# Kernel tuning notes

Measured on AMD Instinct MI355X. Metric: run time of the kernel, lower is better.

## Reference

```python
import jax, jax.numpy as jnp
import numpy as np

N = 50000
E = 800000
F_IN = 128
HID = 128
NCLS = 40


def setup_inputs() -> dict:
    key = jax.random.key(0)
    ks = jax.random.split(key, 12)
    def glorot(k, fan_in, fan_out):
        s = jnp.sqrt(6.0 / (fan_in + fan_out))
        return jax.random.uniform(k, (fan_in, fan_out), jnp.float32, -s, s)
    x = jax.random.normal(ks[0], (N, F_IN), jnp.float32)
    edge_index = jax.random.randint(ks[1], (2, E), 0, N, jnp.int64)
    W1 = glorot(ks[2], F_IN, HID); b1 = jnp.zeros((HID,), jnp.float32)
    W2 = glorot(ks[3], HID, HID);  b2 = jnp.zeros((HID,), jnp.float32)
    W3 = glorot(ks[4], HID, HID);  b3 = jnp.zeros((HID,), jnp.float32)
    Wc = glorot(ks[5], HID, NCLS)
    bc = jnp.zeros((NCLS,), jnp.float32)
    return {"x": x, "edge_index": edge_index, "W1": W1, "b1": b1,
            "W2": W2, "b2": b2, "W3": W3, "b3": b3, "Wc": Wc, "bc": bc}


def _gcn_conv(h, src, dst, norm, W, b):
    # GCNConv: linear transform, then normalized scatter-add aggregation
    h = h @ W                              # [N, out]
    msg = h[src] * norm[:, None]           # [E+N, out] gathered + scaled
    out = jax.ops.segment_sum(msg, dst, num_segments=N)
    return out + b


def reference(x, edge_index, W1, b1, W2, b2, W3, b3, Wc, bc):
    # add self-loops (PyG GCNConv default) and compute symmetric norm once
    loop = jnp.arange(N, dtype=edge_index.dtype)
    src = jnp.concatenate([edge_index[0], loop])
    dst = jnp.concatenate([edge_index[1], loop])
    deg = jax.ops.segment_sum(jnp.ones_like(dst, dtype=x.dtype), dst, num_segments=N)
    dinv = jax.lax.rsqrt(deg)              # deg >= 1 due to self-loops
    norm = dinv[src] * dinv[dst]           # [E+N]

    h = jax.nn.relu(_gcn_conv(x, src, dst, norm, W1, b1))
    h = jax.nn.relu(_gcn_conv(h, src, dst, norm, W2, b2))
    h = jax.nn.relu(_gcn_conv(h, src, dst, norm, W3, b3))
    out = h @ Wc + bc
    return (out, h)
```

## Files before the change

kernel.cpp:

```cpp
#include <hip/hip_runtime.h>
#include <hip/hip_fp16.h>


#define FEAT 128

typedef _Float16 half_t;
typedef _Float16 f16x8 __attribute__((ext_vector_type(8)));
typedef float f32x16 __attribute__((ext_vector_type(16)));


__global__ __launch_bounds__(256) void k_prep(const float* __restrict__ W1,
                                              const float* __restrict__ W2,
                                              const float* __restrict__ W3,
                                              half_t* __restrict__ Wt1,
                                              half_t* __restrict__ Wt2,
                                              half_t* __restrict__ Wt3,
                                              int* __restrict__ deg, int N) {
  int idx = blockIdx.x * 256 + threadIdx.x;
  if (idx < N) deg[idx] = 0;
  if (idx < 3 * 16384) {
    int which = idx >> 14;
    int i = idx & 16383;
    int k = i >> 7, n = i & 127;
    const float* W = (which == 0) ? W1 : (which == 1) ? W2 : W3;
    half_t* Wt = (which == 0) ? Wt1 : (which == 1) ? Wt2 : Wt3;
    Wt[n * 128 + k] = (half_t)W[i];
  }
}


__global__ __launch_bounds__(256) void k_count_rank(const int* __restrict__ dst,
                                                    int* __restrict__ deg,
                                                    int* __restrict__ rank, int E) {
  int e = blockIdx.x * 256 + threadIdx.x;
  if (e < E) rank[e] = atomicAdd(&deg[dst[e]], 1);
}

__global__ __launch_bounds__(256) void k_scanA(const int* __restrict__ deg,
                                               int* __restrict__ partial, int N) {
  __shared__ int s[256];
  int t = threadIdx.x;
  int i = blockIdx.x * 256 + t;
  s[t] = (i < N) ? deg[i] : 0;
  __syncthreads();
  for (int off = 128; off > 0; off >>= 1) {
    if (t < off) s[t] += s[t + off];
    __syncthreads();
  }
  if (t == 0) partial[blockIdx.x] = s[0];
}

__global__ __launch_bounds__(256) void k_scanB(int* __restrict__ partial, int nblk,
                                               int* __restrict__ offsets, int N) {
  __shared__ int s[256];
  int t = threadIdx.x;
  int v = (t < nblk) ? partial[t] : 0;
  s[t] = v;
  __syncthreads();
  for (int off = 1; off < 256; off <<= 1) {
    int x = (t >= off) ? s[t - off] : 0;
    __syncthreads();
    s[t] += x;
    __syncthreads();
  }
  if (t < nblk) partial[t] = s[t] - v;
  if (t == 0) offsets[N] = s[255];
}

__global__ __launch_bounds__(256) void k_scanC(const int* __restrict__ deg,
                                               const int* __restrict__ partial,
                                               int* __restrict__ offsets,
                                               float* __restrict__ dinv, int N) {
  __shared__ int s[256];
  int t = threadIdx.x;
  int i = blockIdx.x * 256 + t;
  int v = (i < N) ? deg[i] : 0;
  s[t] = v;
  __syncthreads();
  for (int off = 1; off < 256; off <<= 1) {
    int x = (t >= off) ? s[t - off] : 0;
    __syncthreads();
    s[t] += x;
    __syncthreads();
  }
  if (i < N) {
    offsets[i] = partial[blockIdx.x] + s[t] - v;
    dinv[i] = rsqrtf((float)(v + 1));
  }
}

__global__ __launch_bounds__(256) void k_place(const int* __restrict__ src,
                                               const int* __restrict__ dst,
                                               const int* __restrict__ offsets,
                                               const int* __restrict__ rank,
                                               int* __restrict__ col, int E) {
  int e = blockIdx.x * 256 + threadIdx.x;
  if (e < E) col[offsets[dst[e]] + rank[e]] = src[e];
}

template <int SRC_FP32>
__global__ __launch_bounds__(256) void k_gemm_mfma(const void* __restrict__ Asrc,
                                                   const half_t* __restrict__ Wt,
                                                   const float* __restrict__ dinv,
                                                   half_t* __restrict__ T,
                                                   int nrows) {
  __shared__ char lds[65536];
  char* sA = lds;
  char* sW = lds + 32768;
  int t = threadIdx.x;
  int rowBase = blockIdx.x * 128;
  int rowsHere = min(128, nrows - rowBase);

  #pragma unroll
  for (int i = 0; i < 8; ++i) {
    int lin = t + i * 256;
    int r = lin >> 4, c = lin & 15;
    *(float4*)(sW + r * 256 + ((c * 16) ^ ((r & 15) << 4))) =
        *(const float4*)((const char*)Wt + r * 256 + c * 16);
  }
  if (SRC_FP32) {
    const float* Af = (const float*)Asrc;
    #pragma unroll
    for (int i = 0; i < 8; ++i) {
      int lin = t + i * 256;
      int r = lin >> 4, c = lin & 15;
      f16x8 h = {};
      if (r < rowsHere) {
        const float4* p = (const float4*)(Af + (size_t)(rowBase + r) * FEAT + c * 8);
        float4 v0 = p[0], v1 = p[1];
        h[0] = (half_t)v0.x; h[1] = (half_t)v0.y; h[2] = (half_t)v0.z; h[3] = (half_t)v0.w;
        h[4] = (half_t)v1.x; h[5] = (half_t)v1.y; h[6] = (half_t)v1.z; h[7] = (half_t)v1.w;
      }
      *(f16x8*)(sA + r * 256 + ((c * 16) ^ ((r & 15) << 4))) = h;
    }
  } else {
    const char* Ah = (const char*)Asrc;
    #pragma unroll
    for (int i = 0; i < 8; ++i) {
      int lin = t + i * 256;
      int r = lin >> 4, c = lin & 15;
      float4 v = {};
      if (r < rowsHere) v = *(const float4*)(Ah + (size_t)(rowBase + r) * 256 + c * 16);
      *(float4*)(sA + r * 256 + ((c * 16) ^ ((r & 15) << 4))) = v;
    }
  }
  __syncthreads();

  int wv = t >> 6;
  int l = t & 63;
  int l31 = l & 31;
  int lhi = l >> 5;
  int sw = (l31 & 15) << 4;

  f32x16 acc[4] = {};

  #pragma unroll
  for (int step = 0; step < 8; ++step) {
    int ko = (step * 32 + lhi * 16) ^ sw;
    f16x8 a  = *(const f16x8*)(sA + (wv * 32 + l31) * 256 + ko);
    f16x8 b0 = *(const f16x8*)(sW + (l31) * 256 + ko);
    f16x8 b1 = *(const f16x8*)(sW + (32 + l31) * 256 + ko);
    f16x8 b2 = *(const f16x8*)(sW + (64 + l31) * 256 + ko);
    f16x8 b3 = *(const f16x8*)(sW + (96 + l31) * 256 + ko);
    acc[0] = __builtin_amdgcn_mfma_f32_32x32x16_f16(a, b0, acc[0], 0, 0, 0);
    acc[1] = __builtin_amdgcn_mfma_f32_32x32x16_f16(a, b1, acc[1], 0, 0, 0);
    acc[2] = __builtin_amdgcn_mfma_f32_32x32x16_f16(a, b2, acc[2], 0, 0, 0);
    acc[3] = __builtin_amdgcn_mfma_f32_32x32x16_f16(a, b3, acc[3], 0, 0, 0);
  }

  #pragma unroll
  for (int j = 0; j < 16; ++j) {
    int rloc = wv * 32 + (j & 3) + 8 * (j >> 2) + 4 * lhi;
    if (rloc < rowsHere) {
      int grow = rowBase + rloc;
      float d = dinv[grow];
      #pragma unroll
      for (int n = 0; n < 4; ++n) {
        T[(size_t)grow * FEAT + n * 32 + l31] = (half_t)(acc[n][j] * d);
      }
    }
  }
}

template <int OUTF>
__global__ __launch_bounds__(256) void k_aggregate(const uint2* __restrict__ T4,
                                                   const int* __restrict__ offsets,
                                                   const int* __restrict__ col,
                                                   const float* __restrict__ dinv,
                                                   const float* __restrict__ bias,
                                                   float4* __restrict__ outF,
                                                   uint2* __restrict__ outH,
                                                   int N) {
  int wave = threadIdx.x >> 6;
  int half = (threadIdx.x >> 5) & 1;
  int q = threadIdx.x & 31;
  int node = (blockIdx.x * 4 + wave) * 2 + half;
  if (node >= N) return;
  int e0 = offsets[node], e1 = offsets[node + 1];

  uint2 sv = T4[(size_t)node * 32 + q];
  __half2 h0 = *(__half2*)&sv.x, h1 = *(__half2*)&sv.y;
  float ax = __half2float(h0.x), ay = __half2float(h0.y);
  float az = __half2float(h1.x), aw = __half2float(h1.y);

  int e = e0;
  for (; e + 8 <= e1; e += 8) {
    int s0 = col[e + 0], s1 = col[e + 1], s2 = col[e + 2], s3 = col[e + 3];
    int s4 = col[e + 4], s5 = col[e + 5], s6 = col[e + 6], s7 = col[e + 7];
    uint2 v0 = T4[(size_t)s0 * 32 + q];
    uint2 v1 = T4[(size_t)s1 * 32 + q];
    uint2 v2 = T4[(size_t)s2 * 32 + q];
    uint2 v3 = T4[(size_t)s3 * 32 + q];
    uint2 v4 = T4[(size_t)s4 * 32 + q];
    uint2 v5 = T4[(size_t)s5 * 32 + q];
    uint2 v6 = T4[(size_t)s6 * 32 + q];
    uint2 v7 = T4[(size_t)s7 * 32 + q];
    #pragma unroll
    for (int u = 0; u < 8; ++u) {
      uint2 v = (u == 0) ? v0 : (u == 1) ? v1 : (u == 2) ? v2 : (u == 3) ? v3
              : (u == 4) ? v4 : (u == 5) ? v5 : (u == 6) ? v6 : v7;
      __half2 p0 = *(__half2*)&v.x, p1 = *(__half2*)&v.y;
      ax += __half2float(p0.x); ay += __half2float(p0.y);
      az += __half2float(p1.x); aw += __half2float(p1.y);
    }
  }
  for (; e < e1; ++e) {
    uint2 v = T4[(size_t)col[e] * 32 + q];
    __half2 p0 = *(__half2*)&v.x, p1 = *(__half2*)&v.y;
    ax += __half2float(p0.x); ay += __half2float(p0.y);
    az += __half2float(p1.x); aw += __half2float(p1.y);
  }

  float di = dinv[node];
  float4 b = ((const float4*)bias)[q];
  float ox = fmaxf(di * ax + b.x, 0.f);
  float oy = fmaxf(di * ay + b.y, 0.f);
  float oz = fmaxf(di * az + b.z, 0.f);
  float ow = fmaxf(di * aw + b.w, 0.f);
  if (OUTF) {
    outF[(size_t)node * 32 + q] = make_float4(ox, oy, oz, ow);
  } else {
    uint2 o;
    __half2 t0 = __floats2half2_rn(ox, oy), t1 = __floats2half2_rn(oz, ow);
    o.x = *(unsigned*)&t0; o.y = *(unsigned*)&t1;
    outH[(size_t)node * 32 + q] = o;
  }
}

__global__ __launch_bounds__(256) void k_classifier(const float* __restrict__ h,
                                                    const float* __restrict__ Wc,
                                                    const float* __restrict__ bc,
                                                    float* __restrict__ out, int N) {
  __shared__ float sh[64 * 132];
  __shared__ float sWt[40 * 130];
  int t = threadIdx.x;
  int nodeBase = blockIdx.x * 64;
  int nodesHere = min(64, N - nodeBase);

  for (int i = t; i < FEAT * 40; i += 256) {
    int k = i / 40, c = i - k * 40;
    sWt[c * 130 + k] = Wc[i];
  }
  {
    const float4* H4 = (const float4*)(h + (size_t)nodeBase * FEAT);
    #pragma unroll
    for (int i = 0; i < 8; ++i) {
      int lin = t + i * 256;
      int r = lin >> 5, kc = lin & 31;
      float4 v = make_float4(0.f, 0.f, 0.f, 0.f);
      if (r < nodesHere) v = H4[lin];
      *(float4*)&sh[r * 132 + kc * 4] = v;
    }
  }
  __syncthreads();

  int n0 = (t >> 3) * 2;
  int cg = (t & 7) * 5;
  float acc0[5], acc1[5];
  #pragma unroll
  for (int j = 0; j < 5; ++j) { acc0[j] = bc[cg + j]; acc1[j] = acc0[j]; }

  #pragma unroll 4
  for (int k4 = 0; k4 < 32; ++k4) {
    float4 h0 = *(const float4*)&sh[n0 * 132 + k4 * 4];
    float4 h1 = *(const float4*)&sh[(n0 + 1) * 132 + k4 * 4];
    #pragma unroll
    for (int j = 0; j < 5; ++j) {
      float4 w = *(const float4*)&sWt[(cg + j) * 130 + k4 * 4];
      acc0[j] += h0.x * w.x + h0.y * w.y + h0.z * w.z + h0.w * w.w;
      acc1[j] += h1.x * w.x + h1.y * w.y + h1.z * w.z + h1.w * w.w;
    }
  }

  if (n0 < nodesHere) {
    float* o = out + (size_t)(nodeBase + n0) * 40 + cg;
    #pragma unroll
    for (int j = 0; j < 5; ++j) o[j] = acc0[j];
  }
  if (n0 + 1 < nodesHere) {
    float* o = out + (size_t)(nodeBase + n0 + 1) * 40 + cg;
    #pragma unroll
    for (int j = 0; j < 5; ++j) o[j] = acc1[j];
  }
}


extern "C" void kernel_launch(void* const* d_in, const int* in_sizes, int n_in,
                              void* d_out, int out_size, void* d_ws, size_t ws_size,
                              hipStream_t stream) {
  const float* x    = (const float*)d_in[0];
  const int*   edge = (const int*)d_in[1];
  const float* W1   = (const float*)d_in[2];
  const float* b1   = (const float*)d_in[3];
  const float* W2   = (const float*)d_in[4];
  const float* b2   = (const float*)d_in[5];
  const float* W3   = (const float*)d_in[6];
  const float* b3   = (const float*)d_in[7];
  const float* Wc   = (const float*)d_in[8];
  const float* bc   = (const float*)d_in[9];

  int N = in_sizes[0] / FEAT;
  int E = in_sizes[1] / 2;

  float* out  = (float*)d_out;
  float* hOut = out + (size_t)N * 40;

  size_t o = 0;
  char* wsb = (char*)d_ws;
  auto take = [&](size_t bytes) -> void* {
    void* p = wsb + o;
    o += (bytes + 255) & ~(size_t)255;
    return p;
  };
  float*   dinv    = (float*)take((size_t)N * 4);
  int*     deg     = (int*)take((size_t)N * 4);
  int*     rank    = (int*)take((size_t)E * 4);
  int*     partial = (int*)take(256 * 4);
  int*     offsets = (int*)take(((size_t)N + 8) * 4);
  int*     col     = (int*)take((size_t)E * 4);
  half_t*  T2h     = (half_t*)take((size_t)N * FEAT * 2);
  half_t*  Bh      = (half_t*)take((size_t)N * FEAT * 2);
  half_t*  Wt1     = (half_t*)take(16384 * 2);
  half_t*  Wt2     = (half_t*)take(16384 * 2);
  half_t*  Wt3     = (half_t*)take(16384 * 2);

  const int* e_src = edge;
  const int* e_dst = edge + E;

  int nblk = (N + 255) / 256;
  int eblk = (E + 255) / 256;

  k_prep<<<nblk, 256, 0, stream>>>(W1, W2, W3, Wt1, Wt2, Wt3, deg, N);
  k_count_rank<<<eblk, 256, 0, stream>>>(e_dst, deg, rank, E);
  k_scanA<<<nblk, 256, 0, stream>>>(deg, partial, N);
  k_scanB<<<1, 256, 0, stream>>>(partial, nblk, offsets, N);
  k_scanC<<<nblk, 256, 0, stream>>>(deg, partial, offsets, dinv, N);
  k_place<<<eblk, 256, 0, stream>>>(e_src, e_dst, offsets, rank, col, E);

  int gblk = (N + 127) / 128;
  int ablk = (N + 7) / 8;
  uint2* T4 = (uint2*)T2h;
  k_gemm_mfma<1><<<gblk, 256, 0, stream>>>(x, Wt1, dinv, T2h, N);
  k_aggregate<0><<<ablk, 256, 0, stream>>>(T4, offsets, col, dinv, b1, nullptr,
                                           (uint2*)Bh, N);
  k_gemm_mfma<0><<<gblk, 256, 0, stream>>>(Bh, Wt2, dinv, T2h, N);
  k_aggregate<0><<<ablk, 256, 0, stream>>>(T4, offsets, col, dinv, b2, nullptr,
                                           (uint2*)Bh, N);
  k_gemm_mfma<0><<<gblk, 256, 0, stream>>>(Bh, Wt3, dinv, T2h, N);
  k_aggregate<1><<<ablk, 256, 0, stream>>>(T4, offsets, col, dinv, b3,
                                           (float4*)hOut, nullptr, N);
  k_classifier<<<(N + 63) / 64, 256, 0, stream>>>(hOut, Wc, bc, out, N);
}
```

Before: 230.3 us.

## Fuse classifier into last aggregation, widen gather to 16B, merge scan passes

Replaces the single-block scanB with a per-block serial sum of partials inside the final scan kernel, removing one launch. Aggregation now uses 16 lanes per node with 16-byte uint4 loads instead of 32 lanes with 8-byte loads. The classifier is fused into the last aggregation: each block stages Wc in shared memory and computes logits from the fresh h values, so hOut is no longer re-read. The trade-offs are an O(nblk) serial loop per scan block, a Wc staging cost in every aggregation block, and less memory parallelism per node in the gather.

```diff
diff --git a/kernel.cpp b/kernel.cpp
--- a/kernel.cpp
+++ b/kernel.cpp
@@ -50,30 +50,15 @@
   if (t == 0) partial[blockIdx.x] = s[0];
 }
 
-__global__ __launch_bounds__(256) void k_scanB(int* __restrict__ partial, int nblk,
-                                               int* __restrict__ offsets, int N) {
+__global__ __launch_bounds__(256) void k_scanC2(const int* __restrict__ deg,
+                                                const int* __restrict__ partial,
+                                                int* __restrict__ offsets,
+                                                float* __restrict__ dinv, int N) {
   __shared__ int s[256];
   int t = threadIdx.x;
-  int v = (t < nblk) ? partial[t] : 0;
-  s[t] = v;
-  __syncthreads();
-  for (int off = 1; off < 256; off <<= 1) {
-    int x = (t >= off) ? s[t - off] : 0;
-    __syncthreads();
-    s[t] += x;
-    __syncthreads();
-  }
-  if (t < nblk) partial[t] = s[t] - v;
-  if (t == 0) offsets[N] = s[255];
-}
-
-__global__ __launch_bounds__(256) void k_scanC(const int* __restrict__ deg,
-                                               const int* __restrict__ partial,
-                                               int* __restrict__ offsets,
-                                               float* __restrict__ dinv, int N) {
-  __shared__ int s[256];
-  int t = threadIdx.x;
   int i = blockIdx.x * 256 + t;
+  int base = 0;
+  for (int j = 0; j < blockIdx.x; ++j) base += partial[j];
   int v = (i < N) ? deg[i] : 0;
   s[t] = v;
   __syncthreads();
@@ -84,8 +69,9 @@
     __syncthreads();
   }
   if (i < N) {
-    offsets[i] = partial[blockIdx.x] + s[t] - v;
+    offsets[i] = base + s[t] - v;
     dinv[i] = rsqrtf((float)(v + 1));
+    if (i == N - 1) offsets[N] = base + s[t];
   }
 }
 
@@ -182,125 +168,139 @@
   }
 }
 
-template <int OUTF>
-__global__ __launch_bounds__(256) void k_aggregate(const uint2* __restrict__ T4,
+
+__device__ __forceinline__ void acc8(float* a, uint4 v) {
+  __half2 p0 = *(__half2*)&v.x, p1 = *(__half2*)&v.y;
+  __half2 p2 = *(__half2*)&v.z, p3 = *(__half2*)&v.w;
+  a[0] += __half2float(p0.x); a[1] += __half2float(p0.y);
+  a[2] += __half2float(p1.x); a[3] += __half2float(p1.y);
+  a[4] += __half2float(p2.x); a[5] += __half2float(p2.y);
+  a[6] += __half2float(p3.x); a[7] += __half2float(p3.y);
+}
+
+__device__ __forceinline__ void gather_node(const uint4* __restrict__ T8,
+                                            const int* __restrict__ offsets,
+                                            const int* __restrict__ col,
+                                            int node, int q, float* a) {
+  uint4 sv = T8[(size_t)node * 16 + q];
+  __half2 p0 = *(__half2*)&sv.x, p1 = *(__half2*)&sv.y;
+  __half2 p2 = *(__half2*)&sv.z, p3 = *(__half2*)&sv.w;
+  a[0] = __half2float(p0.x); a[1] = __half2float(p0.y);
+  a[2] = __half2float(p1.x); a[3] = __half2float(p1.y);
+  a[4] = __half2float(p2.x); a[5] = __half2float(p2.y);
+  a[6] = __half2float(p3.x); a[7] = __half2float(p3.y);
+
+  int e0 = offsets[node], e1 = offsets[node + 1];
+  int e = e0;
+  for (; e + 8 <= e1; e += 8) {
+    int s[8];
+    uint4 v[8];
+    #pragma unroll
+    for (int u = 0; u < 8; ++u) s[u] = col[e + u];
+    #pragma unroll
+    for (int u = 0; u < 8; ++u) v[u] = T8[(size_t)s[u] * 16 + q];
+    #pragma unroll
+    for (int u = 0; u < 8; ++u) acc8(a, v[u]);
+  }
+  for (; e < e1; ++e) acc8(a, T8[(size_t)col[e] * 16 + q]);
+}
+
+__global__ __launch_bounds__(256) void k_aggregate(const uint4* __restrict__ T8,
                                                    const int* __restrict__ offsets,
                                                    const int* __restrict__ col,
                                                    const float* __restrict__ dinv,
                                                    const float* __restrict__ bias,
-                                                   float4* __restrict__ outF,
-                                                   uint2* __restrict__ outH,
+                                                   uint4* __restrict__ outH,
                                                    int N) {
-  int wave = threadIdx.x >> 6;
-  int half = (threadIdx.x >> 5) & 1;
-  int q = threadIdx.x & 31;
-  int node = (blockIdx.x * 4 + wave) * 2 + half;
+  int t = threadIdx.x;
+  int node = blockIdx.x * 16 + (t >> 4);
+  int q = t & 15;
   if (node >= N) return;
-  int e0 = offsets[node], e1 = offsets[node + 1];
-
-  uint2 sv = T4[(size_t)node * 32 + q];
-  __half2 h0 = *(__half2*)&sv.x, h1 = *(__half2*)&sv.y;
-  float ax = __half2float(h0.x), ay = __half2float(h0.y);
-  float az = __half2float(h1.x), aw = __half2float(h1.y);
-
-  int e = e0;
-  for (; e + 8 <= e1; e += 8) {
-    int s0 = col[e + 0], s1 = col[e + 1], s2 = col[e + 2], s3 = col[e + 3];
-    int s4 = col[e + 4], s5 = col[e + 5], s6 = col[e + 6], s7 = col[e + 7];
-    uint2 v0 = T4[(size_t)s0 * 32 + q];
-    uint2 v1 = T4[(size_t)s1 * 32 + q];
-    uint2 v2 = T4[(size_t)s2 * 32 + q];
-    uint2 v3 = T4[(size_t)s3 * 32 + q];
-    uint2 v4 = T4[(size_t)s4 * 32 + q];
-    uint2 v5 = T4[(size_t)s5 * 32 + q];
-    uint2 v6 = T4[(size_t)s6 * 32 + q];
-    uint2 v7 = T4[(size_t)s7 * 32 + q];
-    #pragma unroll
-    for (int u = 0; u < 8; ++u) {
-      uint2 v = (u == 0) ? v0 : (u == 1) ? v1 : (u == 2) ? v2 : (u == 3) ? v3
-              : (u == 4) ? v4 : (u == 5) ? v5 : (u == 6) ? v6 : v7;
-      __half2 p0 = *(__half2*)&v.x, p1 = *(__half2*)&v.y;
-      ax += __half2float(p0.x); ay += __half2float(p0.y);
-      az += __half2float(p1.x); aw += __half2float(p1.y);
-    }
-  }
-  for (; e < e1; ++e) {
-    uint2 v = T4[(size_t)col[e] * 32 + q];
-    __half2 p0 = *(__half2*)&v.x, p1 = *(__half2*)&v.y;
-    ax += __half2float(p0.x); ay += __half2float(p0.y);
-    az += __half2float(p1.x); aw += __half2float(p1.y);
-  }
+
+  float a[8];
+  gather_node(T8, offsets, col, node, q, a);
 
   float di = dinv[node];
-  float4 b = ((const float4*)bias)[q];
-  float ox = fmaxf(di * ax + b.x, 0.f);
-  float oy = fmaxf(di * ay + b.y, 0.f);
-  float oz = fmaxf(di * az + b.z, 0.f);
-  float ow = fmaxf(di * aw + b.w, 0.f);
-  if (OUTF) {
-    outF[(size_t)node * 32 + q] = make_float4(ox, oy, oz, ow);
-  } else {
-    uint2 o;
-    __half2 t0 = __floats2half2_rn(ox, oy), t1 = __floats2half2_rn(oz, ow);
-    o.x = *(unsigned*)&t0; o.y = *(unsigned*)&t1;
-    outH[(size_t)node * 32 + q] = o;
-  }
-}
-
-__global__ __launch_bounds__(256) void k_classifier(const float* __restrict__ h,
-                                                    const float* __restrict__ Wc,
-                                                    const float* __restrict__ bc,
-                                                    float* __restrict__ out, int N) {
-  __shared__ float sh[64 * 132];
-  __shared__ float sWt[40 * 130];
-  int t = threadIdx.x;
-  int nodeBase = blockIdx.x * 64;
-  int nodesHere = min(64, N - nodeBase);
-
+  const float4* b4 = (const float4*)bias;
+  float4 bA = b4[2 * q], bB = b4[2 * q + 1];
+  float o0 = fmaxf(di * a[0] + bA.x, 0.f);
+  float o1 = fmaxf(di * a[1] + bA.y, 0.f);
+  float o2 = fmaxf(di * a[2] + bA.z, 0.f);
+  float o3 = fmaxf(di * a[3] + bA.w, 0.f);
+  float o4 = fmaxf(di * a[4] + bB.x, 0.f);
+  float o5 = fmaxf(di * a[5] + bB.y, 0.f);
+  float o6 = fmaxf(di * a[6] + bB.z, 0.f);
+  float o7 = fmaxf(di * a[7] + bB.w, 0.f);
+
+  __half2 h0 = __floats2half2_rn(o0, o1), h1 = __floats2half2_rn(o2, o3);
+  __half2 h2 = __floats2half2_rn(o4, o5), h3 = __floats2half2_rn(o6, o7);
+  uint4 o;
+  o.x = *(unsigned*)&h0; o.y = *(unsigned*)&h1;
+  o.z = *(unsigned*)&h2; o.w = *(unsigned*)&h3;
+  outH[(size_t)node * 16 + q] = o;
+}
+
+__global__ __launch_bounds__(256) void k_aggregate_cls(const uint4* __restrict__ T8,
+                                                       const int* __restrict__ offsets,
+                                                       const int* __restrict__ col,
+                                                       const float* __restrict__ dinv,
+                                                       const float* __restrict__ bias,
+                                                       const float* __restrict__ Wc,
+                                                       const float* __restrict__ bc,
+                                                       float* __restrict__ logits,
+                                                       float4* __restrict__ hOut,
+                                                       int N) {
+  __shared__ float sWcT[40 * 132];
+  __shared__ float sh[16 * 132];
+  int t = threadIdx.x;
   for (int i = t; i < FEAT * 40; i += 256) {
     int k = i / 40, c = i - k * 40;
-    sWt[c * 130 + k] = Wc[i];
-  }
-  {
-    const float4* H4 = (const float4*)(h + (size_t)nodeBase * FEAT);
-    #pragma unroll
-    for (int i = 0; i < 8; ++i) {
-      int lin = t + i * 256;
-      int r = lin >> 5, kc = lin & 31;
-      float4 v = make_float4(0.f, 0.f, 0.f, 0.f);
-      if (r < nodesHere) v = H4[lin];
-      *(float4*)&sh[r * 132 + kc * 4] = v;
+    sWcT[c * 132 + k] = Wc[i];
+  }
+  __syncthreads();
+
+  int node = blockIdx.x * 16 + (t >> 4);
+  int q = t & 15;
+  if (node < N) {
+    float a[8];
+    gather_node(T8, offsets, col, node, q, a);
+
+    float di = dinv[node];
+    const float4* b4 = (const float4*)bias;
+    float4 bA = b4[2 * q], bB = b4[2 * q + 1];
+    float4 oA, oB;
+    oA.x = fmaxf(di * a[0] + bA.x, 0.f);
+    oA.y = fmaxf(di * a[1] + bA.y, 0.f);
+    oA.z = fmaxf(di * a[2] + bA.z, 0.f);
+    oA.w = fmaxf(di * a[3] + bA.w, 0.f);
+    oB.x = fmaxf(di * a[4] + bB.x, 0.f);
+    oB.y = fmaxf(di * a[5] + bB.y, 0.f);
+    oB.z = fmaxf(di * a[6] + bB.z, 0.f);
+    oB.w = fmaxf(di * a[7] + bB.w, 0.f);
+
+    hOut[(size_t)node * 32 + 2 * q] = oA;
+    hOut[(size_t)node * 32 + 2 * q + 1] = oB;
+
+    int loc = t >> 4;
+    *(float4*)&sh[loc * 132 + 8 * q] = oA;
+    *(float4*)&sh[loc * 132 + 8 * q + 4] = oB;
+
+    const float4* hv = (const float4*)&sh[loc * 132];
+    #pragma unroll
+    for (int j = 0; j < 3; ++j) {
+      int c = q + 16 * j;
+      if (c < 40) {
+        const float4* wv = (const float4*)&sWcT[c * 132];
+        float acc = bc[c];
+        #pragma unroll 8
+        for (int k4 = 0; k4 < 32; ++k4) {
+          float4 hh = hv[k4];
+          float4 ww = wv[k4];
+          acc += hh.x * ww.x + hh.y * ww.y + hh.z * ww.z + hh.w * ww.w;
+        }
+        logits[(size_t)node * 40 + c] = acc;
+      }
     }
-  }
-  __syncthreads();
-
-  int n0 = (t >> 3) * 2;
-  int cg = (t & 7) * 5;
-  float acc0[5], acc1[5];
-  #pragma unroll
-  for (int j = 0; j < 5; ++j) { acc0[j] = bc[cg + j]; acc1[j] = acc0[j]; }
-
-  #pragma unroll 4
-  for (int k4 = 0; k4 < 32; ++k4) {
-    float4 h0 = *(const float4*)&sh[n0 * 132 + k4 * 4];
-    float4 h1 = *(const float4*)&sh[(n0 + 1) * 132 + k4 * 4];
-    #pragma unroll
-    for (int j = 0; j < 5; ++j) {
-      float4 w = *(const float4*)&sWt[(cg + j) * 130 + k4 * 4];
-      acc0[j] += h0.x * w.x + h0.y * w.y + h0.z * w.z + h0.w * w.w;
-      acc1[j] += h1.x * w.x + h1.y * w.y + h1.z * w.z + h1.w * w.w;
-    }
-  }
-
-  if (n0 < nodesHere) {
-    float* o = out + (size_t)(nodeBase + n0) * 40 + cg;
-    #pragma unroll
-    for (int j = 0; j < 5; ++j) o[j] = acc0[j];
-  }
-  if (n0 + 1 < nodesHere) {
-    float* o = out + (size_t)(nodeBase + n0 + 1) * 40 + cg;
-    #pragma unroll
-    for (int j = 0; j < 5; ++j) o[j] = acc1[j];
   }
 }
 
@@ -353,21 +353,17 @@
   k_prep<<<nblk, 256, 0, stream>>>(W1, W2, W3, Wt1, Wt2, Wt3, deg, N);
   k_count_rank<<<eblk, 256, 0, stream>>>(e_dst, deg, rank, E);
   k_scanA<<<nblk, 256, 0, stream>>>(deg, partial, N);
-  k_scanB<<<1, 256, 0, stream>>>(partial, nblk, offsets, N);
-  k_scanC<<<nblk, 256, 0, stream>>>(deg, partial, offsets, dinv, N);
+  k_scanC2<<<nblk, 256, 0, stream>>>(deg, partial, offsets, dinv, N);
   k_place<<<eblk, 256, 0, stream>>>(e_src, e_dst, offsets, rank, col, E);
 
   int gblk = (N + 127) / 128;
-  int ablk = (N + 7) / 8;
-  uint2* T4 = (uint2*)T2h;
+  int ablk = (N + 15) / 16;
+  uint4* T8 = (uint4*)T2h;
   k_gemm_mfma<1><<<gblk, 256, 0, stream>>>(x, Wt1, dinv, T2h, N);
-  k_aggregate<0><<<ablk, 256, 0, stream>>>(T4, offsets, col, dinv, b1, nullptr,
-                                           (uint2*)Bh, N);
+  k_aggregate<<<ablk, 256, 0, stream>>>(T8, offsets, col, dinv, b1, (uint4*)Bh, N);
   k_gemm_mfma<0><<<gblk, 256, 0, stream>>>(Bh, Wt2, dinv, T2h, N);
-  k_aggregate<0><<<ablk, 256, 0, stream>>>(T4, offsets, col, dinv, b2, nullptr,
-                                           (uint2*)Bh, N);
+  k_aggregate<<<ablk, 256, 0, stream>>>(T8, offsets, col, dinv, b2, (uint4*)Bh, N);
   k_gemm_mfma<0><<<gblk, 256, 0, stream>>>(Bh, Wt3, dinv, T2h, N);
-  k_aggregate<1><<<ablk, 256, 0, stream>>>(T4, offsets, col, dinv, b3,
-                                           (float4*)hOut, nullptr, N);
-  k_classifier<<<(N + 63) / 64, 256, 0, stream>>>(hOut, Wc, bc, out, N);
-}
+  k_aggregate_cls<<<ablk, 256, 0, stream>>>(T8, offsets, col, dinv, b3, Wc, bc,
+                                            out, (float4*)hOut, N);
+}
```

Result: no change. 232.2 us (+0.8%).
